# Kernel tuning notes

Measured on AMD Instinct MI355X. Metric: run time of the kernel, lower is better.

The kernel has to match this reference:

```python
import jax, jax.numpy as jnp
import numpy as np

N = 131072
UNITS = 256
GAMMA_RBF = 0.5  # 1 / sigma2, sigma2 = 2


def setup_inputs() -> dict:
    key = jax.random.key(0)
    ks = jax.random.split(key, 6)
    x = jax.random.uniform(ks[0], (N, 1), dtype=jnp.float32)
    y = jax.random.uniform(ks[1], (N, 1), dtype=jnp.float32)
    u = jax.random.normal(ks[2], (N, 1), dtype=jnp.float32)
    centers = jax.random.uniform(ks[3], (UNITS, 2), dtype=jnp.float32)
    W = jax.random.normal(ks[4], (UNITS, 1), dtype=jnp.float32) * 0.05
    epsilon = jnp.array([0.5], dtype=jnp.float32)
    delta = jnp.array([0.406], dtype=jnp.float32)
    gamma = jnp.array([0.196], dtype=jnp.float32)
    return {"x": x, "y": y, "u": u, "centers": centers, "W": W,
            "epsilon": epsilon, "delta": delta, "gamma": gamma,
            "iterations": 40000}


def reference(x, y, u, centers, W, epsilon, delta, gamma, iterations):
    # scalar RBF net: u(x,y) = sum_j W_j * exp(-gamma_rbf * ||(x,y) - c_j||^2)
    w = W[:, 0]
    cx, cy = centers[:, 0], centers[:, 1]

    def u_scalar(xi, yi):
        d2 = (xi - cx) ** 2 + (yi - cy) ** 2  # [UNITS]
        return jnp.exp(-GAMMA_RBF * d2) @ w    # scalar

    # second derivatives
    u_xx = jax.grad(jax.grad(u_scalar, 0), 0)
    u_yy = jax.grad(jax.grad(u_scalar, 1), 1)

    def lap_fn(xi, yi):
        return u_xx(xi, yi) + u_yy(xi, yi)

    lap_xx = jax.grad(jax.grad(lap_fn, 0), 0)
    lap_yy = jax.grad(jax.grad(lap_fn, 1), 1)

    def bih_fn(xi, yi):
        return lap_xx(xi, yi) + lap_yy(xi, yi)

    xf, yf = x[:, 0], y[:, 0]
    u_pred = jax.vmap(u_scalar)(xf, yf)[:, None]      # [N,1]
    laplace_u = jax.vmap(lap_fn)(xf, yf)[:, None]     # [N,1]
    biharmonic_u = jax.vmap(bih_fn)(xf, yf)[:, None]  # [N,1]

    sh_operator = u_pred + 2.0 * laplace_u + biharmonic_u

    # curriculum schedule on a static Python int
    if iterations < 10000:
        pde_residual = epsilon * u_pred - sh_operator
        cw = 0.1
    elif iterations < 20000:
        pde_residual = epsilon * u_pred - 0.3 * delta * jnp.square(u_pred) - sh_operator
        cw = 0.3
    elif iterations < 30000:
        pde_residual = (epsilon * u_pred - 0.7 * delta * jnp.square(u_pred)
                        - 0.3 * gamma * u_pred ** 3 - sh_operator)
        cw = 0.6
    else:
        pde_residual = (epsilon * u_pred - delta * jnp.square(u_pred)
                        - gamma * u_pred ** 3 - sh_operator)
        cw = 1.0

    loss_u = jnp.mean(jnp.square(u_pred - u)) / jnp.mean(jnp.square(u))
    loss_pde_u = jnp.mean(jnp.square(pde_residual))

    eps_bp = (jnp.maximum(0.0, epsilon - 0.8) ** 2
              + jnp.maximum(0.0, 0.2 - epsilon) ** 2)  # [1]
    weight_pde_u = 1.0
    loss1 = 0.1 * loss_u + cw * weight_pde_u * loss_pde_u + 0.01 * eps_bp  # [1]

    return jnp.concatenate([loss1, loss_u[None], loss_pde_u[None]])  # [3]
```

## Files before the change

kernel.cpp:

```cpp
#include <hip/hip_runtime.h>
#include <math.h>

#define N_PTS 131072
#define UNITS 256
#define BLOCK 256
#define GRID  (N_PTS / BLOCK)

__global__ __launch_bounds__(BLOCK) void rbf_pinn_main(
    const float* __restrict__ x, const float* __restrict__ y,
    const float* __restrict__ u, const float* __restrict__ centers,
    const float* __restrict__ W, const float* __restrict__ eps,
    const float* __restrict__ delta, const float* __restrict__ gam,
    const int* __restrict__ iters, float* __restrict__ partial)
{
    __shared__ float s_cx[UNITS], s_cy[UNITS], s_w[UNITS];
    const int t = threadIdx.x;
    s_cx[t] = centers[2 * t + 0];
    s_cy[t] = centers[2 * t + 1];
    s_w[t]  = W[t];
    __syncthreads();

    const int i = blockIdx.x * BLOCK + t;
    const float xi = x[i];
    const float yi = y[i];
    const float ui = u[i];

    float up = 0.f;
    float sh = 0.f;
    const float c = -0.72134752044448170368f;

    #pragma unroll 8
    for (int j = 0; j < UNITS; ++j) {
        float dx = xi - s_cx[j];
        float dy = yi - s_cy[j];
        float s  = fmaf(dy, dy, dx * dx);
        float e  = __builtin_amdgcn_exp2f(c * s);
        float ew = e * s_w[j];
        up += ew;
        float poly = fmaf(s, s - 6.f, 5.f);
        sh = fmaf(ew, poly, sh);
    }

    const int   it   = iters[0];
    const float epsv = eps[0];
    const float dl   = delta[0];
    const float gm   = gam[0];
    float c2, c3;
    if (it < 10000)      { c2 = 0.0f; c3 = 0.0f; }
    else if (it < 20000) { c2 = 0.3f; c3 = 0.0f; }
    else if (it < 30000) { c2 = 0.7f; c3 = 0.3f; }
    else                 { c2 = 1.0f; c3 = 1.0f; }

    const float up2 = up * up;
    const float res = epsv * up - c2 * dl * up2 - c3 * gm * up2 * up - sh;
    const float d   = up - ui;

    float a0 = d * d;
    float a1 = ui * ui;
    float a2 = res * res;

    #pragma unroll
    for (int o = 32; o > 0; o >>= 1) {
        a0 += __shfl_down(a0, o);
        a1 += __shfl_down(a1, o);
        a2 += __shfl_down(a2, o);
    }
    __shared__ float s_r[3][BLOCK / 64];
    const int lane = t & 63;
    const int wv   = t >> 6;
    if (lane == 0) { s_r[0][wv] = a0; s_r[1][wv] = a1; s_r[2][wv] = a2; }
    __syncthreads();
    if (t == 0) {
        float r0 = 0.f, r1 = 0.f, r2 = 0.f;
        #pragma unroll
        for (int w2 = 0; w2 < BLOCK / 64; ++w2) {
            r0 += s_r[0][w2]; r1 += s_r[1][w2]; r2 += s_r[2][w2];
        }
        partial[0 * GRID + blockIdx.x] = r0;
        partial[1 * GRID + blockIdx.x] = r1;
        partial[2 * GRID + blockIdx.x] = r2;
    }
}

__global__ __launch_bounds__(256) void rbf_pinn_final(
    const float* __restrict__ partial, const float* __restrict__ eps,
    const int* __restrict__ iters, float* __restrict__ out)
{
    const int t = threadIdx.x;
    float a0 = 0.f, a1 = 0.f, a2 = 0.f;
    for (int k = t; k < GRID; k += 256) {
        a0 += partial[0 * GRID + k];
        a1 += partial[1 * GRID + k];
        a2 += partial[2 * GRID + k];
    }
    #pragma unroll
    for (int o = 32; o > 0; o >>= 1) {
        a0 += __shfl_down(a0, o);
        a1 += __shfl_down(a1, o);
        a2 += __shfl_down(a2, o);
    }
    __shared__ float s_r[3][4];
    const int lane = t & 63;
    const int wv   = t >> 6;
    if (lane == 0) { s_r[0][wv] = a0; s_r[1][wv] = a1; s_r[2][wv] = a2; }
    __syncthreads();
    if (t == 0) {
        float S0 = 0.f, S1 = 0.f, S2 = 0.f;
        #pragma unroll
        for (int w2 = 0; w2 < 4; ++w2) { S0 += s_r[0][w2]; S1 += s_r[1][w2]; S2 += s_r[2][w2]; }
        const float loss_u   = S0 / S1;
        const float loss_pde = S2 / (float)N_PTS;
        const int it = iters[0];
        float cw;
        if (it < 10000)      cw = 0.1f;
        else if (it < 20000) cw = 0.3f;
        else if (it < 30000) cw = 0.6f;
        else                 cw = 1.0f;
        const float e = eps[0];
        const float b0 = fmaxf(0.f, e - 0.8f);
        const float b1 = fmaxf(0.f, 0.2f - e);
        const float eps_bp = b0 * b0 + b1 * b1;
        const float loss1 = 0.1f * loss_u + cw * loss_pde + 0.01f * eps_bp;
        out[0] = loss1;
        out[1] = loss_u;
        out[2] = loss_pde;
    }
}

extern "C" void kernel_launch(void* const* d_in, const int* in_sizes, int n_in,
                              void* d_out, int out_size, void* d_ws, size_t ws_size,
                              hipStream_t stream) {
    const float* x       = (const float*)d_in[0];
    const float* y       = (const float*)d_in[1];
    const float* u       = (const float*)d_in[2];
    const float* centers = (const float*)d_in[3];
    const float* W       = (const float*)d_in[4];
    const float* eps     = (const float*)d_in[5];
    const float* delta   = (const float*)d_in[6];
    const float* gam     = (const float*)d_in[7];
    const int*   iters   = (const int*)d_in[8];
    float* out = (float*)d_out;
    float* partial = (float*)d_ws;

    rbf_pinn_main<<<GRID, BLOCK, 0, stream>>>(x, y, u, centers, W, eps, delta,
                                              gam, iters, partial);
    rbf_pinn_final<<<1, 256, 0, stream>>>(partial, eps, iters, out);
}
```

Baseline: 19.64 us.

## Precompute expanded RBF coefficients and fuse final reduction via last-block atomic

Expands the squared distance into per-center linear coefficients stored as float4 in shared memory, so each inner iteration needs fewer ALU ops and one LDS load. The polynomial in the distance is rewritten in terms of the exponent argument. The separate finalize kernel is replaced by a last-block-done atomic counter pattern, with a memset to reset the counter. Expanding the distance algebraically can lose some floating-point precision through cancellation, and the memset adds its own stream operation.

```diff
diff --git a/kernel.cpp b/kernel.cpp
--- a/kernel.cpp
+++ b/kernel.cpp
@@ -6,38 +6,50 @@
 #define BLOCK 256
 #define GRID  (N_PTS / BLOCK)
 
-__global__ __launch_bounds__(BLOCK) void rbf_pinn_main(
+__global__ __launch_bounds__(BLOCK) void rbf_pinn_fused(
     const float* __restrict__ x, const float* __restrict__ y,
     const float* __restrict__ u, const float* __restrict__ centers,
     const float* __restrict__ W, const float* __restrict__ eps,
     const float* __restrict__ delta, const float* __restrict__ gam,
-    const int* __restrict__ iters, float* __restrict__ partial)
+    const int* __restrict__ iters, float* __restrict__ partial,
+    unsigned int* __restrict__ counter, float* __restrict__ out)
 {
-    __shared__ float s_cx[UNITS], s_cy[UNITS], s_w[UNITS];
+    __shared__ float4 s_coef[UNITS];
     const int t = threadIdx.x;
-    s_cx[t] = centers[2 * t + 0];
-    s_cy[t] = centers[2 * t + 1];
-    s_w[t]  = W[t];
+    const float c = -0.72134752044448170368f;
+
+    {
+        const float cx = centers[2 * t + 0];
+        const float cy = centers[2 * t + 1];
+        const float w  = W[t];
+        const float A  = -2.f * c * cx;
+        const float B  = -2.f * c * cy;
+        const float D  = c * fmaf(cx, cx, cy * cy);
+        s_coef[t] = make_float4(A, B, D, w);
+    }
     __syncthreads();
 
     const int i = blockIdx.x * BLOCK + t;
     const float xi = x[i];
     const float yi = y[i];
     const float ui = u[i];
+    const float tb = c * fmaf(xi, xi, yi * yi);
+
+    const float ic2  = 1.9218120556728056f;
+    const float m6ic = 8.3187661667193446f;
 
     float up = 0.f;
     float sh = 0.f;
-    const float c = -0.72134752044448170368f;
 
     #pragma unroll 8
     for (int j = 0; j < UNITS; ++j) {
-        float dx = xi - s_cx[j];
-        float dy = yi - s_cy[j];
-        float s  = fmaf(dy, dy, dx * dx);
-        float e  = __builtin_amdgcn_exp2f(c * s);
-        float ew = e * s_w[j];
+        const float4 cf = s_coef[j];
+        const float tt = fmaf(cf.x, xi, fmaf(cf.y, yi, tb + cf.z));
+        const float e  = __builtin_amdgcn_exp2f(tt);
+        const float ew = e * cf.w;
         up += ew;
-        float poly = fmaf(s, s - 6.f, 5.f);
+        const float u1   = fmaf(ic2, tt, m6ic);
+        const float poly = fmaf(tt, u1, 5.f);
         sh = fmaf(ew, poly, sh);
     }
 
@@ -70,6 +82,8 @@
     const int wv   = t >> 6;
     if (lane == 0) { s_r[0][wv] = a0; s_r[1][wv] = a1; s_r[2][wv] = a2; }
     __syncthreads();
+
+    __shared__ bool s_last;
     if (t == 0) {
         float r0 = 0.f, r1 = 0.f, r2 = 0.f;
         #pragma unroll
@@ -79,49 +93,47 @@
         partial[0 * GRID + blockIdx.x] = r0;
         partial[1 * GRID + blockIdx.x] = r1;
         partial[2 * GRID + blockIdx.x] = r2;
+        __threadfence();
+        const unsigned old = atomicAdd(counter, 1u);
+        s_last = (old == GRID - 1);
     }
-}
+    __syncthreads();
+    if (!s_last) return;
 
-__global__ __launch_bounds__(256) void rbf_pinn_final(
-    const float* __restrict__ partial, const float* __restrict__ eps,
-    const int* __restrict__ iters, float* __restrict__ out)
-{
-    const int t = threadIdx.x;
-    float a0 = 0.f, a1 = 0.f, a2 = 0.f;
-    for (int k = t; k < GRID; k += 256) {
-        a0 += partial[0 * GRID + k];
-        a1 += partial[1 * GRID + k];
-        a2 += partial[2 * GRID + k];
+    __threadfence();
+    float b0 = 0.f, b1 = 0.f, b2 = 0.f;
+    #pragma unroll
+    for (int k = t; k < GRID; k += BLOCK) {
+        b0 += partial[0 * GRID + k];
+        b1 += partial[1 * GRID + k];
+        b2 += partial[2 * GRID + k];
     }
     #pragma unroll
     for (int o = 32; o > 0; o >>= 1) {
-        a0 += __shfl_down(a0, o);
-        a1 += __shfl_down(a1, o);
-        a2 += __shfl_down(a2, o);
+        b0 += __shfl_down(b0, o);
+        b1 += __shfl_down(b1, o);
+        b2 += __shfl_down(b2, o);
     }
-    __shared__ float s_r[3][4];
-    const int lane = t & 63;
-    const int wv   = t >> 6;
-    if (lane == 0) { s_r[0][wv] = a0; s_r[1][wv] = a1; s_r[2][wv] = a2; }
+    if (lane == 0) { s_r[0][wv] = b0; s_r[1][wv] = b1; s_r[2][wv] = b2; }
     __syncthreads();
     if (t == 0) {
         float S0 = 0.f, S1 = 0.f, S2 = 0.f;
         #pragma unroll
-        for (int w2 = 0; w2 < 4; ++w2) { S0 += s_r[0][w2]; S1 += s_r[1][w2]; S2 += s_r[2][w2]; }
+        for (int w2 = 0; w2 < BLOCK / 64; ++w2) {
+            S0 += s_r[0][w2]; S1 += s_r[1][w2]; S2 += s_r[2][w2];
+        }
         const float loss_u   = S0 / S1;
         const float loss_pde = S2 / (float)N_PTS;
-        const int it = iters[0];
         float cw;
         if (it < 10000)      cw = 0.1f;
         else if (it < 20000) cw = 0.3f;
         else if (it < 30000) cw = 0.6f;
         else                 cw = 1.0f;
-        const float e = eps[0];
-        const float b0 = fmaxf(0.f, e - 0.8f);
-        const float b1 = fmaxf(0.f, 0.2f - e);
-        const float eps_bp = b0 * b0 + b1 * b1;
-        const float loss1 = 0.1f * loss_u + cw * loss_pde + 0.01f * eps_bp;
-        out[0] = loss1;
+        const float e  = epsv;
+        const float p0 = fmaxf(0.f, e - 0.8f);
+        const float p1 = fmaxf(0.f, 0.2f - e);
+        const float eps_bp = p0 * p0 + p1 * p1;
+        out[0] = 0.1f * loss_u + cw * loss_pde + 0.01f * eps_bp;
         out[1] = loss_u;
         out[2] = loss_pde;
     }
@@ -140,9 +152,11 @@
     const float* gam     = (const float*)d_in[7];
     const int*   iters   = (const int*)d_in[8];
     float* out = (float*)d_out;
+
     float* partial = (float*)d_ws;
+    unsigned int* counter = (unsigned int*)((char*)d_ws + 8192);
 
-    rbf_pinn_main<<<GRID, BLOCK, 0, stream>>>(x, y, u, centers, W, eps, delta,
-                                              gam, iters, partial);
-    rbf_pinn_final<<<1, 256, 0, stream>>>(partial, eps, iters, out);
+    hipMemsetAsync(counter, 0, sizeof(unsigned int), stream);
+    rbf_pinn_fused<<<GRID, BLOCK, 0, stream>>>(x, y, u, centers, W, eps, delta,
+                                               gam, iters, partial, counter, out);
 }
```

Measured after the change: 30.26 us. 54.1% more time.

## Factor RBF exponent into per-point and linear per-center terms, pair centers

Applied to the files above, without the earlier changes.

Expands the squared distance in the RBF exponent so each center contributes a linear form in (x,y) plus a precomputed constant, and pulls the per-point exp factor out of the sum. The Swift-Hohenberg polynomial is rewritten in terms of the new exponent argument with precomputed coefficients. Centers are packed as float4 pairs in shared memory with dual accumulators to cut per-center ALU work and LDS loads. This risks precision loss from cancellation in the expanded exponent.

```diff
diff --git a/kernel.cpp b/kernel.cpp
--- a/kernel.cpp
+++ b/kernel.cpp
@@ -3,8 +3,10 @@
 
 #define N_PTS 131072
 #define UNITS 256
+#define PAIRS (UNITS / 2)
 #define BLOCK 256
 #define GRID  (N_PTS / BLOCK)
+
 
 __global__ __launch_bounds__(BLOCK) void rbf_pinn_main(
     const float* __restrict__ x, const float* __restrict__ y,
@@ -13,11 +15,28 @@
     const float* __restrict__ delta, const float* __restrict__ gam,
     const int* __restrict__ iters, float* __restrict__ partial)
 {
-    __shared__ float s_cx[UNITS], s_cy[UNITS], s_w[UNITS];
+    constexpr double LOG2E = 1.4426950408889634073599;
+    constexpr float  cF    = (float)(-0.5 * LOG2E);
+    constexpr float  alpha = (float)(1.0 / (0.25 * LOG2E * LOG2E));
+    constexpr float  m2c   = (float)(2.0 / (-0.5 * LOG2E));
+    constexpr float  m6c   = (float)(-6.0 / (-0.5 * LOG2E));
+
+    __shared__ float4 s_ab[PAIRS];
+    __shared__ float4 s_dw[PAIRS];
     const int t = threadIdx.x;
-    s_cx[t] = centers[2 * t + 0];
-    s_cy[t] = centers[2 * t + 1];
-    s_w[t]  = W[t];
+
+    if (t < PAIRS) {
+        const float cx0 = centers[4 * t + 0];
+        const float cy0 = centers[4 * t + 1];
+        const float cx1 = centers[4 * t + 2];
+        const float cy1 = centers[4 * t + 3];
+        const float w0  = W[2 * t + 0];
+        const float w1  = W[2 * t + 1];
+        s_ab[t] = make_float4(-2.f * cF * cx0, -2.f * cF * cx1,
+                              -2.f * cF * cy0, -2.f * cF * cy1);
+        s_dw[t] = make_float4(cF * fmaf(cx0, cx0, cy0 * cy0),
+                              cF * fmaf(cx1, cx1, cy1 * cy1), w0, w1);
+    }
     __syncthreads();
 
     const int i = blockIdx.x * BLOCK + t;
@@ -25,21 +44,35 @@
     const float yi = y[i];
     const float ui = u[i];
 
-    float up = 0.f;
-    float sh = 0.f;
-    const float c = -0.72134752044448170368f;
+    const float r0   = fmaf(xi, xi, yi * yi);
+    const float E0   = __builtin_amdgcn_exp2f(cF * r0);
+    const float beta = fmaf(m2c, r0, m6c);
+    const float gmma = fmaf(r0, r0 - 6.f, 5.f);
 
-    #pragma unroll 8
-    for (int j = 0; j < UNITS; ++j) {
-        float dx = xi - s_cx[j];
-        float dy = yi - s_cy[j];
-        float s  = fmaf(dy, dy, dx * dx);
-        float e  = __builtin_amdgcn_exp2f(c * s);
-        float ew = e * s_w[j];
-        up += ew;
-        float poly = fmaf(s, s - 6.f, 5.f);
-        sh = fmaf(ew, poly, sh);
+    float up0 = 0.f, up1 = 0.f;
+    float sh0 = 0.f, sh1 = 0.f;
+
+    #pragma unroll 4
+    for (int p = 0; p < PAIRS; ++p) {
+        const float4 ab = s_ab[p];
+        const float4 dw = s_dw[p];
+        const float q0 = fmaf(ab.x, xi, fmaf(ab.z, yi, dw.x));
+        const float q1 = fmaf(ab.y, xi, fmaf(ab.w, yi, dw.y));
+        const float e0 = __builtin_amdgcn_exp2f(q0);
+        const float e1 = __builtin_amdgcn_exp2f(q1);
+        const float p10 = fmaf(alpha, q0, beta);
+        const float p11 = fmaf(alpha, q1, beta);
+        const float pl0 = fmaf(q0, p10, gmma);
+        const float pl1 = fmaf(q1, p11, gmma);
+        const float ew0 = e0 * dw.z;
+        const float ew1 = e1 * dw.w;
+        up0 += ew0;
+        up1 += ew1;
+        sh0 = fmaf(ew0, pl0, sh0);
+        sh1 = fmaf(ew1, pl1, sh1);
     }
+    const float up = (up0 + up1) * E0;
+    const float sh = (sh0 + sh1) * E0;
 
     const int   it   = iters[0];
     const float epsv = eps[0];
@@ -71,14 +104,14 @@
     if (lane == 0) { s_r[0][wv] = a0; s_r[1][wv] = a1; s_r[2][wv] = a2; }
     __syncthreads();
     if (t == 0) {
-        float r0 = 0.f, r1 = 0.f, r2 = 0.f;
+        float r0s = 0.f, r1s = 0.f, r2s = 0.f;
         #pragma unroll
         for (int w2 = 0; w2 < BLOCK / 64; ++w2) {
-            r0 += s_r[0][w2]; r1 += s_r[1][w2]; r2 += s_r[2][w2];
+            r0s += s_r[0][w2]; r1s += s_r[1][w2]; r2s += s_r[2][w2];
         }
-        partial[0 * GRID + blockIdx.x] = r0;
-        partial[1 * GRID + blockIdx.x] = r1;
-        partial[2 * GRID + blockIdx.x] = r2;
+        partial[0 * GRID + blockIdx.x] = r0s;
+        partial[1 * GRID + blockIdx.x] = r1s;
+        partial[2 * GRID + blockIdx.x] = r2s;
     }
 }
 
@@ -88,6 +121,7 @@
 {
     const int t = threadIdx.x;
     float a0 = 0.f, a1 = 0.f, a2 = 0.f;
+    #pragma unroll
     for (int k = t; k < GRID; k += 256) {
         a0 += partial[0 * GRID + k];
         a1 += partial[1 * GRID + k];
@@ -116,12 +150,11 @@
         else if (it < 20000) cw = 0.3f;
         else if (it < 30000) cw = 0.6f;
         else                 cw = 1.0f;
-        const float e = eps[0];
-        const float b0 = fmaxf(0.f, e - 0.8f);
-        const float b1 = fmaxf(0.f, 0.2f - e);
-        const float eps_bp = b0 * b0 + b1 * b1;
-        const float loss1 = 0.1f * loss_u + cw * loss_pde + 0.01f * eps_bp;
-        out[0] = loss1;
+        const float e  = eps[0];
+        const float p0 = fmaxf(0.f, e - 0.8f);
+        const float p1 = fmaxf(0.f, 0.2f - e);
+        const float eps_bp = p0 * p0 + p1 * p1;
+        out[0] = 0.1f * loss_u + cw * loss_pde + 0.01f * eps_bp;
         out[1] = loss_u;
         out[2] = loss_pde;
     }
```

Measured after the change: 17.92 us. 1.1x faster.
